# Kernel optimization log

Measured on AMD Instinct MI355X. Metric: run time of the kernel, lower is better.

The kernel has to match this reference:

```python
import jax, jax.numpy as jnp
import numpy as np
from jax import lax

T = 8
TAU = 2.0
V_TH = 1.0
V_RESET = 0.0
ALPHA = 2.0  # ATan surrogate width


@jax.custom_vjp
def spike(x):
    # Heaviside forward, ATan surrogate backward (spikingjelly surrogate.ATan)
    return (x >= 0.0).astype(x.dtype)

def _spike_fwd(x):
    return spike(x), x

def _spike_bwd(x, g):
    pi_half_alpha = jnp.asarray(np.pi / 2.0 * ALPHA, x.dtype)
    grad = (ALPHA / 2.0) / (1.0 + (pi_half_alpha * x) ** 2)
    return (g * grad,)

spike.defvjp(_spike_fwd, _spike_bwd)


def lif_multistep(x_seq):
    # x_seq: [T, ...]; hard-reset LIF with decay_input=True:
    #   v <- v + (x - (v - v_reset)) / tau ; s = H(v - v_th) ; v <- (1-s)*v + s*v_reset
    v0 = jnp.full(x_seq.shape[1:], V_RESET, x_seq.dtype)
    def step(v, x):
        v = v + (x - (v - V_RESET)) / TAU
        s = spike(v - V_TH)
        v = (1.0 - s) * v + s * V_RESET
        return v, s
    _, s_seq = lax.scan(step, v0, x_seq)
    return s_seq


def conv2d(x, w, b, stride):
    y = lax.conv_general_dilated(x, w, (stride, stride), 'VALID',
                                 dimension_numbers=('NCHW', 'OIHW', 'NCHW'))
    return y + b[None, :, None, None]


def seq_conv(x_seq, w, b, stride):
    # SeqToANNContainer: fold T into batch, run conv, unfold
    t, bsz = x_seq.shape[0], x_seq.shape[1]
    y = conv2d(x_seq.reshape((t * bsz,) + x_seq.shape[2:]), w, b, stride)
    return y.reshape((t, bsz) + y.shape[1:])


def setup_inputs() -> dict:
    key = jax.random.key(0)
    ks = jax.random.split(key, 12)
    s = 0.05
    return {
        'x':    jax.random.normal(ks[0], (512, 4, 84, 84), jnp.float32),
        'w1':   jax.random.normal(ks[1], (32, 4, 8, 8), jnp.float32) * s,
        'b1':   jax.random.normal(ks[2], (32,), jnp.float32) * s,
        'w2':   jax.random.normal(ks[3], (64, 32, 4, 4), jnp.float32) * s,
        'b2':   jax.random.normal(ks[4], (64,), jnp.float32) * s,
        'w3':   jax.random.normal(ks[5], (64, 64, 3, 3), jnp.float32) * s,
        'b3':   jax.random.normal(ks[6], (64,), jnp.float32) * s,
        'fw1':  jax.random.normal(ks[7], (512, 64 * 7 * 7), jnp.float32) * s,
        'fb1':  jax.random.normal(ks[8], (512,), jnp.float32) * s,
        'fw2':  jax.random.normal(ks[9], (6, 512), jnp.float32) * s,
        'fb2':  jax.random.normal(ks[10], (6,), jnp.float32) * s,
    }


def reference(x, w1, b1, w2, b2, w3, b3, fw1, fb1, fw2, fb2):
    # static conv, then replicate across T timesteps
    h = conv2d(x, w1, b1, 4)                      # [B,32,20,20]
    x_seq = jnp.broadcast_to(h[None], (T,) + h.shape)
    s = lif_multistep(x_seq)                      # [T,B,32,20,20]
    s = lif_multistep(seq_conv(s, w2, b2, 2))     # [T,B,64,9,9]
    s = lif_multistep(seq_conv(s, w3, b3, 1))     # [T,B,64,7,7]
    flat = s.reshape(T, s.shape[1], -1)           # [T,B,3136]
    s = lif_multistep(jnp.einsum('tbi,oi->tbo', flat, fw1) + fb1)  # [T,B,512]
    out = s.mean(axis=0)                          # [B,512]
    return out @ fw2.T + fb2                      # [B,6]
```

## Files before the change

### kernel.cpp

```cpp
#include <hip/hip_runtime.h>
#include <cstdint>

#define RFL(x) __builtin_amdgcn_readfirstlane(x)

static constexpr int B  = 512;
static constexpr int C0 = 4,  H0 = 84, W0 = 84;
static constexpr int C1 = 32, H1 = 20, W1 = 20, P1 = H1 * W1;
static constexpr int C2 = 64, H2 = 9,  W2 = 9,  P2 = H2 * W2;
static constexpr int C3 = 64, H3 = 7,  W3 = 7,  P3 = H3 * W3;
static constexpr int K  = C3 * P3;
static constexpr int O  = 512;
static constexpr int NJOB2 = B * P2;

static constexpr size_t OFF_S1   = 0;
static constexpr size_t OFF_S2   = 6553600;
static constexpr size_t OFF_S3   = OFF_S2 + 2654208;
static constexpr size_t OFF_W2T  = OFF_S3 + 1605632;
static constexpr size_t OFF_W3T  = OFF_W2T + 131072 + 256;
static constexpr size_t OFF_FW1T = OFF_W3T + 147456;
static constexpr size_t OFF_W1T  = OFF_FW1T + 6422528;
static constexpr size_t OFF_CNT  = OFF_W1T + 32768;
static constexpr size_t OFF_EVT  = OFF_CNT + (size_t)NJOB2 * 32;
static constexpr size_t WS_NEEDED = OFF_EVT + (size_t)NJOB2 * 1088;

__global__ void k_prep_w1(const float* __restrict__ w1, float* __restrict__ w1T) {
    int n = blockIdx.x * 256 + threadIdx.x;
    if (n >= 8192) return;
    int kx = n & 7, o = (n >> 3) & 7, ky = (n >> 6) & 7, ic = (n >> 9) & 3, o8 = n >> 11;
    int oc = o8 * 8 + o;
    w1T[n] = w1[((oc * 4 + ic) * 8 + ky) * 8 + kx];
}

__global__ void k_prep_w2(const float* __restrict__ w2, float* __restrict__ w2T) {
    int idx = blockIdx.x * 256 + threadIdx.x;
    if (idx >= 32768) {
        if (idx < 32768 + 64) w2T[idx] = 0.0f;
        return;
    }
    int oc = idx >> 9, r = idx & 511;
    int ic = r >> 4, ky = (r >> 2) & 3, kx = r & 3;
    w2T[((ky * 4 + kx) * 32 + ic) * 64 + oc] = w2[idx];
}

__global__ void k_prep_w3(const float* __restrict__ w3, float* __restrict__ w3T) {
    int idx = blockIdx.x * 256 + threadIdx.x;
    if (idx >= 64 * 64 * 9) return;
    int oc = idx / 576, r = idx - oc * 576;
    int ic = r / 9, rr = r - ic * 9;
    int ky = rr / 3, kx = rr - ky * 3;
    w3T[((ky * 3 + kx) * 64 + ic) * 64 + oc] = w3[idx];
}

__global__ __launch_bounds__(256) void k_prep_fw1(const float* __restrict__ fw1,
                                                  float* __restrict__ fw1T) {
    __shared__ float tile[64][65];
    int ot = blockIdx.x & 7;
    int it = blockIdx.x >> 3;
    int tr = threadIdx.x >> 6;
    int tc = threadIdx.x & 63;
    #pragma unroll
    for (int r = 0; r < 16; r++) {
        int ol = r * 4 + tr;
        tile[ol][tc] = fw1[(size_t)(ot * 64 + ol) * K + it * 64 + tc];
    }
    __syncthreads();
    #pragma unroll
    for (int r = 0; r < 16; r++) {
        int il = r * 4 + tr;
        fw1T[(size_t)(it * 64 + il) * O + ot * 64 + tc] = tile[tc][il];
    }
}

__global__ __launch_bounds__(256) void k_conv1(const float* __restrict__ x,
                                               const float* __restrict__ w1T,
                                               const float* __restrict__ b1,
                                               uint8_t* __restrict__ s1c) {
    int blk = blockIdx.x;
    int o8  = blk / 400;
    int rest = (blk - o8 * 400) * 256 + threadIdx.x;
    int img = rest / 200, pair = rest - img * 200;
    int oy  = pair / 10;
    int ox0 = (pair - oy * 10) * 2;
    const float* xb = x + (size_t)img * 28224 + (size_t)(oy * 4) * W0 + ox0 * 4;
    const float* wh = w1T + o8 * 2048;

    float acc[2][8];
    #pragma unroll
    for (int pp = 0; pp < 2; pp++)
        #pragma unroll
        for (int o = 0; o < 8; o++) acc[pp][o] = b1[o8 * 8 + o];

    #pragma unroll 1
    for (int ic = 0; ic < C0; ic++) {
        #pragma unroll 1
        for (int ky = 0; ky < 8; ky++) {
            const float* rp = xb + ic * 7056 + ky * W0;
            float4 a0 = *(const float4*)rp;
            float4 a1 = *(const float4*)(rp + 4);
            float4 a2 = *(const float4*)(rp + 8);
            float xv[12] = {a0.x, a0.y, a0.z, a0.w, a1.x, a1.y, a1.z, a1.w,
                            a2.x, a2.y, a2.z, a2.w};
            const float* wb = wh + (ic * 8 + ky) * 64;
            #pragma unroll
            for (int o = 0; o < 8; o++) {
                #pragma unroll
                for (int pp = 0; pp < 2; pp++) {
                    float s = acc[pp][o];
                    #pragma unroll
                    for (int kx = 0; kx < 8; kx++)
                        s = fmaf(wb[o * 8 + kx], xv[pp * 4 + kx], s);
                    acc[pp][o] = s;
                }
            }
        }
    }

    #pragma unroll
    for (int pp = 0; pp < 2; pp++) {
        uint32_t byc[8] = {0, 0, 0, 0, 0, 0, 0, 0};
        #pragma unroll
        for (int o = 0; o < 8; o++) {
            float h = acc[pp][o], v = 0.f;
            uint32_t mm = 0;
            #pragma unroll
            for (int t = 0; t < 8; t++) {
                v = v + (h - v) * 0.5f;
                bool sp = (v >= 1.0f);
                mm |= sp ? (1u << t) : 0u;
                v = sp ? 0.f : v;
            }
            uint32_t fs = mm & (0u - mm);
            #pragma unroll
            for (int c = 0; c < 8; c++) byc[c] |= ((fs >> c) & 1u) << o;
        }
        int pix = oy * W1 + ox0 + pp;
        uint8_t* op = s1c + (size_t)(img * P1 + pix) * 32 + o8;
        #pragma unroll
        for (int c = 0; c < 8; c++) op[c * 4] = (uint8_t)byc[c];
    }
}

__global__ __launch_bounds__(256) void k_evt(const uint8_t* __restrict__ s1c,
                                             uint32_t* __restrict__ cnt,
                                             uint16_t* __restrict__ evl) {
    int job = blockIdx.x * 256 + threadIdx.x;
    if (job >= NJOB2) return;
    int b = job / P2, pix = job - b * P2;
    int oy = pix / W2, ox = pix - oy * W2;
    uint16_t* out = evl + (size_t)job * 544;
    int k = 0;
    #pragma unroll 1
    for (int c = 0; c < 8; c++) {
        int start = k;
        #pragma unroll 1
        for (int pos = 0; pos < 16; pos++) {
            int ky = pos >> 2, kx = pos & 3;
            int ipix = (oy * 2 + ky) * W1 + ox * 2 + kx;
            uint32_t w = *(const uint32_t*)(s1c + (size_t)(b * P1 + ipix) * 32 + c * 4);
            while (w) {
                int i = __builtin_ctz(w);
                w &= w - 1;
                out[k++] = (uint16_t)((pos << 5) + i);
            }
        }
        while ((k - start) & 3) out[k++] = 512;
        cnt[job * 8 + c] = (uint32_t)(k - start);
    }
}

__global__ __launch_bounds__(256) void k_conv2_ev(const uint32_t* __restrict__ cnt,
                                                  const uint16_t* __restrict__ evl,
                                                  const float* __restrict__ w2T,
                                                  const float* __restrict__ b2,
                                                  uint8_t* __restrict__ s2p) {
    int wid = RFL(blockIdx.x * 4 + (threadIdx.x >> 6));
    int lane = threadIdx.x & 63;
    int b = wid / P2, pix = wid - b * P2;
    const uint32_t* evw = (const uint32_t*)(evl + (size_t)wid * 544);
    const uint32_t* cp  = cnt + wid * 8;
    float A[8];
    #pragma unroll
    for (int c = 0; c < 8; c++) A[c] = 0.f;
    int kw = 0;
    #define CLS(c)                                                            \
    {   int n = (int)cp[c];                                                   \
        for (int k = 0; k < n; k += 4) {                                      \
            uint32_t d0 = evw[kw], d1 = evw[kw + 1]; kw += 2;                 \
            float v0 = w2T[(d0 & 0xffffu) * 64 + lane];                       \
            float v1 = w2T[(d0 >> 16)    * 64 + lane];                        \
            float v2 = w2T[(d1 & 0xffffu) * 64 + lane];                       \
            float v3 = w2T[(d1 >> 16)    * 64 + lane];                        \
            A[c] += v0; A[c] += v1; A[c] += v2; A[c] += v3;                   \
        }                                                                     \
    }
    CLS(0) CLS(1) CLS(2) CLS(3) CLS(4) CLS(5) CLS(6) CLS(7)
    #undef CLS

    float y[8];
    y[0] = A[0];
    y[1] = A[0] + A[1];
    y[2] = A[0] + A[2];
    y[3] = A[0] + A[1] + A[3];
    y[4] = A[0] + A[4];
    y[5] = A[0] + A[1] + A[2] + A[5];
    y[6] = A[0] + A[6];
    y[7] = A[0] + A[1] + A[3] + A[7];

    float bo = b2[lane];
    uint32_t mout = 0;
    float v = 0.f;
    #pragma unroll
    for (int t = 0; t < 8; t++) {
        float yt = y[t] + bo;
        v = v + (yt - v) * 0.5f;
        bool sp = (v >= 1.0f);
        mout |= sp ? (1u << t) : 0u;
        v = sp ? 0.f : v;
    }
    unsigned long long* op = (unsigned long long*)(s2p + (size_t)(b * P2 + pix) * 64);
    #pragma unroll
    for (int t = 0; t < 8; t++) {
        unsigned long long bm = __ballot((mout >> t) & 1u);
        if (lane == 0) op[t] = bm;
    }
}

__global__ __launch_bounds__(256) void k_conv2_old(const uint8_t* __restrict__ s1c,
                                                   const float* __restrict__ w2T,
                                                   const float* __restrict__ b2,
                                                   uint8_t* __restrict__ s2p) {
    int wid = blockIdx.x * 4 + (threadIdx.x >> 6);
    int lane = threadIdx.x & 63;
    int b = wid / P2, pix = wid - b * P2;
    int oy = pix / W2, ox = pix - oy * W2;
    float A[8];
    #pragma unroll
    for (int c = 0; c < 8; c++) A[c] = 0.f;
    #pragma unroll
    for (int ky = 0; ky < 4; ky++) {
        #pragma unroll
        for (int kx = 0; kx < 4; kx++) {
            int mofs = RFL((b * P1 + (oy * 2 + ky) * W1 + (ox * 2 + kx)) * 32);
            const uint32_t* mp = (const uint32_t*)(s1c + mofs);
            const float* wp = w2T + (ky * 4 + kx) * 32 * 64 + lane;
            uint32_t w0 = mp[0], w1 = mp[1], w2 = mp[2], w3 = mp[3];
            uint32_t w4 = mp[4], w5 = mp[5], w6 = mp[6], w7 = mp[7];
            while (w0 | w1 | w2 | w3 | w4 | w5 | w6 | w7) {
                if (w0) { int i = __builtin_ctz(w0); w0 &= w0 - 1; A[0] += wp[i * 64]; }
                if (w1) { int i = __builtin_ctz(w1); w1 &= w1 - 1; A[1] += wp[i * 64]; }
                if (w2) { int i = __builtin_ctz(w2); w2 &= w2 - 1; A[2] += wp[i * 64]; }
                if (w3) { int i = __builtin_ctz(w3); w3 &= w3 - 1; A[3] += wp[i * 64]; }
                if (w4) { int i = __builtin_ctz(w4); w4 &= w4 - 1; A[4] += wp[i * 64]; }
                if (w5) { int i = __builtin_ctz(w5); w5 &= w5 - 1; A[5] += wp[i * 64]; }
                if (w6) { int i = __builtin_ctz(w6); w6 &= w6 - 1; A[6] += wp[i * 64]; }
                if (w7) { int i = __builtin_ctz(w7); w7 &= w7 - 1; A[7] += wp[i * 64]; }
            }
        }
    }
    float y[8];
    y[0] = A[0];
    y[1] = A[0] + A[1];
    y[2] = A[0] + A[2];
    y[3] = A[0] + A[1] + A[3];
    y[4] = A[0] + A[4];
    y[5] = A[0] + A[1] + A[2] + A[5];
    y[6] = A[0] + A[6];
    y[7] = A[0] + A[1] + A[3] + A[7];
    float bo = b2[lane];
    uint32_t mout = 0;
    float v = 0.f;
    #pragma unroll
    for (int t = 0; t < 8; t++) {
        float yt = y[t] + bo;
        v = v + (yt - v) * 0.5f;
        bool sp = (v >= 1.0f);
        mout |= sp ? (1u << t) : 0u;
        v = sp ? 0.f : v;
    }
    unsigned long long* op = (unsigned long long*)(s2p + (size_t)(b * P2 + pix) * 64);
    #pragma unroll
    for (int t = 0; t < 8; t++) {
        unsigned long long bm = __ballot((mout >> t) & 1u);
        if (lane == 0) op[t] = bm;
    }
}

__global__ __launch_bounds__(256) void k_conv3(const uint8_t* __restrict__ s2p,
                                               const float* __restrict__ w3T,
                                               const float* __restrict__ b3,
                                               uint8_t* __restrict__ s3m) {
    int wid = blockIdx.x * 4 + (threadIdx.x >> 6);
    int lane = threadIdx.x & 63;
    int b = wid / P3, pix = wid - b * P3;
    int oy = pix / W3, ox = pix - oy * W3;
    float A[8];
    #pragma unroll
    for (int t = 0; t < 8; t++) A[t] = 0.f;
    #pragma unroll
    for (int ky = 0; ky < 3; ky++) {
        #pragma unroll
        for (int kx = 0; kx < 3; kx++) {
            int mofs = RFL((b * P2 + (oy + ky) * W2 + (ox + kx)) * 64);
            const unsigned long long* mp = (const unsigned long long*)(s2p + mofs);
            const float* wp = w3T + (ky * 3 + kx) * 64 * 64 + lane;
            unsigned long long m0 = mp[0], m1 = mp[1], m2 = mp[2], m3 = mp[3];
            unsigned long long m4 = mp[4], m5 = mp[5], m6 = mp[6], m7 = mp[7];
            while (m0 | m1 | m2 | m3 | m4 | m5 | m6 | m7) {
                if (m0) { int i = __builtin_ctzll(m0); m0 &= m0 - 1; A[0] += wp[i * 64]; }
                if (m1) { int i = __builtin_ctzll(m1); m1 &= m1 - 1; A[1] += wp[i * 64]; }
                if (m2) { int i = __builtin_ctzll(m2); m2 &= m2 - 1; A[2] += wp[i * 64]; }
                if (m3) { int i = __builtin_ctzll(m3); m3 &= m3 - 1; A[3] += wp[i * 64]; }
                if (m4) { int i = __builtin_ctzll(m4); m4 &= m4 - 1; A[4] += wp[i * 64]; }
                if (m5) { int i = __builtin_ctzll(m5); m5 &= m5 - 1; A[5] += wp[i * 64]; }
                if (m6) { int i = __builtin_ctzll(m6); m6 &= m6 - 1; A[6] += wp[i * 64]; }
                if (m7) { int i = __builtin_ctzll(m7); m7 &= m7 - 1; A[7] += wp[i * 64]; }
            }
        }
    }
    float bo = b3[lane];
    uint32_t mout = 0;
    float v = 0.f;
    #pragma unroll
    for (int t = 0; t < 8; t++) {
        float y = A[t] + bo;
        v = v + (y - v) * 0.5f;
        bool sp = (v >= 1.0f);
        mout |= sp ? (1u << t) : 0u;
        v = sp ? 0.f : v;
    }
    s3m[(size_t)(b * P3 + pix) * 64 + lane] = (uint8_t)mout;
}

__global__ __launch_bounds__(256) void k_fc(const uint8_t* __restrict__ s3m,
                                            const float* __restrict__ fw1T,
                                            const float* __restrict__ fb1,
                                            const float* __restrict__ fw2,
                                            const float* __restrict__ fb2,
                                            float* __restrict__ out) {
    __shared__ float red[3][64][65];
    int b = blockIdx.x;
    int w = threadIdx.x >> 6;
    int lane = threadIdx.x & 63;
    float acc[8][8];
    #pragma unroll
    for (int j = 0; j < 8; j++)
        #pragma unroll
        for (int t = 0; t < 8; t++) acc[j][t] = 0.f;

    int ibeg = w * 784;
    for (int i0 = ibeg; i0 < ibeg + 784; i0 += 16) {
        int base = RFL(b * K + i0);
        const uint32_t* mp = (const uint32_t*)(s3m + base);
        #pragma unroll
        for (int d = 0; d < 4; d++) {
            uint32_t md = mp[d];
            if (md == 0) continue;
            #pragma unroll
            for (int q = 0; q < 4; q++) {
                uint32_t m = (md >> (q * 8)) & 0xffu;
                if (m == 0) continue;
                int i_our = i0 + d * 4 + q;
                int pix = i_our >> 6, c = i_our & 63;
                const float4* wp = (const float4*)(fw1T + (size_t)(c * 49 + pix) * O + lane * 8);
                float4 wa = wp[0], wb = wp[1];
                float wv[8] = {wa.x, wa.y, wa.z, wa.w, wb.x, wb.y, wb.z, wb.w};
                #pragma unroll
                for (int t = 0; t < 8; t++) {
                    if (m & (1u << t)) {
                        #pragma unroll
                        for (int j = 0; j < 8; j++) acc[j][t] += wv[j];
                    }
                }
            }
        }
    }

    if (w > 0) {
        #pragma unroll
        for (int j = 0; j < 8; j++)
            #pragma unroll
            for (int t = 0; t < 8; t++) red[w - 1][lane][j * 8 + t] = acc[j][t];
    }
    __syncthreads();
    if (w != 0) return;

    #pragma unroll
    for (int ww = 0; ww < 3; ww++)
        #pragma unroll
        for (int j = 0; j < 8; j++)
            #pragma unroll
            for (int t = 0; t < 8; t++) acc[j][t] += red[ww][lane][j * 8 + t];

    float msum[8];
    #pragma unroll
    for (int j = 0; j < 8; j++) {
        float yb = fb1[lane * 8 + j];
        float v = 0.f, cntt = 0.f;
        #pragma unroll
        for (int t = 0; t < 8; t++) {
            float y = acc[j][t] + yb;
            v = v + (y - v) * 0.5f;
            bool sp = (v >= 1.0f);
            cntt += sp ? 1.f : 0.f;
            v = sp ? 0.f : v;
        }
        msum[j] = cntt * 0.125f;
    }
    #pragma unroll
    for (int kk = 0; kk < 6; kk++) {
        const float* wr = fw2 + kk * O + lane * 8;
        float pv = 0.f;
        #pragma unroll
        for (int j = 0; j < 8; j++) pv += msum[j] * wr[j];
        #pragma unroll
        for (int off = 32; off > 0; off >>= 1) pv += __shfl_down(pv, off, 64);
        if (lane == 0) out[b * 6 + kk] = pv + fb2[kk];
    }
}

extern "C" void kernel_launch(void* const* d_in, const int* in_sizes, int n_in,
                              void* d_out, int out_size, void* d_ws, size_t ws_size,
                              hipStream_t stream) {
    const float* x   = (const float*)d_in[0];
    const float* w1  = (const float*)d_in[1];
    const float* b1  = (const float*)d_in[2];
    const float* w2  = (const float*)d_in[3];
    const float* b2  = (const float*)d_in[4];
    const float* w3  = (const float*)d_in[5];
    const float* b3  = (const float*)d_in[6];
    const float* fw1 = (const float*)d_in[7];
    const float* fb1 = (const float*)d_in[8];
    const float* fw2 = (const float*)d_in[9];
    const float* fb2 = (const float*)d_in[10];
    float* out = (float*)d_out;

    uint8_t*  ws   = (uint8_t*)d_ws;
    uint8_t*  s1c  = ws + OFF_S1;
    uint8_t*  s2p  = ws + OFF_S2;
    uint8_t*  s3m  = ws + OFF_S3;
    float*    w2T  = (float*)(ws + OFF_W2T);
    float*    w3T  = (float*)(ws + OFF_W3T);
    float*    fw1T = (float*)(ws + OFF_FW1T);
    float*    w1T  = (float*)(ws + OFF_W1T);
    uint32_t* cnt  = (uint32_t*)(ws + OFF_CNT);
    uint16_t* evl  = (uint16_t*)(ws + OFF_EVT);

    hipLaunchKernelGGL(k_prep_w1,  dim3(32),    dim3(256), 0, stream, w1, w1T);
    hipLaunchKernelGGL(k_prep_w2,  dim3(129),   dim3(256), 0, stream, w2, w2T);
    hipLaunchKernelGGL(k_prep_w3,  dim3(144),   dim3(256), 0, stream, w3, w3T);
    hipLaunchKernelGGL(k_prep_fw1, dim3(392),   dim3(256), 0, stream, fw1, fw1T);
    hipLaunchKernelGGL(k_conv1,    dim3(1600),  dim3(256), 0, stream, x, w1T, b1, s1c);
    if (ws_size >= WS_NEEDED) {
        hipLaunchKernelGGL(k_evt,      dim3(162),   dim3(256), 0, stream, s1c, cnt, evl);
        hipLaunchKernelGGL(k_conv2_ev, dim3(10368), dim3(256), 0, stream, cnt, evl, w2T, b2, s2p);
    } else {
        hipLaunchKernelGGL(k_conv2_old, dim3(10368), dim3(256), 0, stream, s1c, w2T, b2, s2p);
    }
    hipLaunchKernelGGL(k_conv3,    dim3(6272),  dim3(256), 0, stream, s2p, w3T, b3, s3m);
    hipLaunchKernelGGL(k_fc,       dim3(512),   dim3(256), 0, stream, s3m, fw1T, fb1, fw2, fb2, out);
}
```

Measured before the change: 194.4 us.

## Parallelize event-list build across channel groups and unroll conv2 gather by eight

The event-list builder now gives each of the 8 channel groups of an output pixel its own thread. Each thread first popcounts its spikes, then uses a segmented shuffle prefix sum to find its write offset, and launches 8x more blocks. Groups are padded to multiples of 8 instead of 4, so the conv2 event kernel can issue 8 weight gathers per iteration for more memory-level parallelism. The per-job event buffer grows, and the extra padding adds wasted dummy gathers against a zero row.

```diff
diff --git a/kernel.cpp b/kernel.cpp
--- a/kernel.cpp
+++ b/kernel.cpp
@@ -21,7 +21,7 @@
 static constexpr size_t OFF_W1T  = OFF_FW1T + 6422528;
 static constexpr size_t OFF_CNT  = OFF_W1T + 32768;
 static constexpr size_t OFF_EVT  = OFF_CNT + (size_t)NJOB2 * 32;
-static constexpr size_t WS_NEEDED = OFF_EVT + (size_t)NJOB2 * 1088;
+static constexpr size_t WS_NEEDED = OFF_EVT + (size_t)NJOB2 * 1152;
 
 __global__ void k_prep_w1(const float* __restrict__ w1, float* __restrict__ w1T) {
     int n = blockIdx.x * 256 + threadIdx.x;
@@ -143,29 +143,42 @@
 __global__ __launch_bounds__(256) void k_evt(const uint8_t* __restrict__ s1c,
                                              uint32_t* __restrict__ cnt,
                                              uint16_t* __restrict__ evl) {
-    int job = blockIdx.x * 256 + threadIdx.x;
-    if (job >= NJOB2) return;
+    int tid = threadIdx.x;
+    int job = blockIdx.x * 32 + (tid >> 3);
+    int c   = tid & 7;
     int b = job / P2, pix = job - b * P2;
     int oy = pix / W2, ox = pix - oy * W2;
-    uint16_t* out = evl + (size_t)job * 544;
+    const uint8_t* sb = s1c + (size_t)b * P1 * 32 + c * 4;
+
+    int count = 0;
+    #pragma unroll
+    for (int pos = 0; pos < 16; pos++) {
+        int ipix = (oy * 2 + (pos >> 2)) * W1 + ox * 2 + (pos & 3);
+        count += __popc(*(const uint32_t*)(sb + (size_t)ipix * 32));
+    }
+    int padded = (count + 7) & ~7;
+
+    int incl = padded;
+    #pragma unroll
+    for (int d = 1; d < 8; d <<= 1) {
+        int t = __shfl_up(incl, d, 8);
+        if ((tid & 7) >= d) incl += t;
+    }
+    uint16_t* out = evl + (size_t)job * 576 + (incl - padded);
+
     int k = 0;
     #pragma unroll 1
-    for (int c = 0; c < 8; c++) {
-        int start = k;
-        #pragma unroll 1
-        for (int pos = 0; pos < 16; pos++) {
-            int ky = pos >> 2, kx = pos & 3;
-            int ipix = (oy * 2 + ky) * W1 + ox * 2 + kx;
-            uint32_t w = *(const uint32_t*)(s1c + (size_t)(b * P1 + ipix) * 32 + c * 4);
-            while (w) {
-                int i = __builtin_ctz(w);
-                w &= w - 1;
-                out[k++] = (uint16_t)((pos << 5) + i);
-            }
-        }
-        while ((k - start) & 3) out[k++] = 512;
-        cnt[job * 8 + c] = (uint32_t)(k - start);
-    }
+    for (int pos = 0; pos < 16; pos++) {
+        int ipix = (oy * 2 + (pos >> 2)) * W1 + ox * 2 + (pos & 3);
+        uint32_t w = *(const uint32_t*)(sb + (size_t)ipix * 32);
+        while (w) {
+            int i = __builtin_ctz(w);
+            w &= w - 1;
+            out[k++] = (uint16_t)((pos << 5) + i);
+        }
+    }
+    while (k < padded) out[k++] = 512;
+    cnt[job * 8 + c] = (uint32_t)padded;
 }
 
 __global__ __launch_bounds__(256) void k_conv2_ev(const uint32_t* __restrict__ cnt,
@@ -176,7 +189,7 @@
     int wid = RFL(blockIdx.x * 4 + (threadIdx.x >> 6));
     int lane = threadIdx.x & 63;
     int b = wid / P2, pix = wid - b * P2;
-    const uint32_t* evw = (const uint32_t*)(evl + (size_t)wid * 544);
+    const uint32_t* evw = (const uint32_t*)(evl + (size_t)wid * 576);
     const uint32_t* cp  = cnt + wid * 8;
     float A[8];
     #pragma unroll
@@ -184,13 +197,19 @@
     int kw = 0;
     #define CLS(c)                                                            \
     {   int n = (int)cp[c];                                                   \
-        for (int k = 0; k < n; k += 4) {                                      \
-            uint32_t d0 = evw[kw], d1 = evw[kw + 1]; kw += 2;                 \
+        for (int k = 0; k < n; k += 8) {                                      \
+            uint32_t d0 = evw[kw], d1 = evw[kw + 1];                          \
+            uint32_t d2 = evw[kw + 2], d3 = evw[kw + 3]; kw += 4;             \
             float v0 = w2T[(d0 & 0xffffu) * 64 + lane];                       \
             float v1 = w2T[(d0 >> 16)    * 64 + lane];                        \
             float v2 = w2T[(d1 & 0xffffu) * 64 + lane];                       \
             float v3 = w2T[(d1 >> 16)    * 64 + lane];                        \
+            float v4 = w2T[(d2 & 0xffffu) * 64 + lane];                       \
+            float v5 = w2T[(d2 >> 16)    * 64 + lane];                        \
+            float v6 = w2T[(d3 & 0xffffu) * 64 + lane];                       \
+            float v7 = w2T[(d3 >> 16)    * 64 + lane];                        \
             A[c] += v0; A[c] += v1; A[c] += v2; A[c] += v3;                   \
+            A[c] += v4; A[c] += v5; A[c] += v6; A[c] += v7;                   \
         }                                                                     \
     }
     CLS(0) CLS(1) CLS(2) CLS(3) CLS(4) CLS(5) CLS(6) CLS(7)
@@ -451,7 +470,7 @@
     hipLaunchKernelGGL(k_prep_fw1, dim3(392),   dim3(256), 0, stream, fw1, fw1T);
     hipLaunchKernelGGL(k_conv1,    dim3(1600),  dim3(256), 0, stream, x, w1T, b1, s1c);
     if (ws_size >= WS_NEEDED) {
-        hipLaunchKernelGGL(k_evt,      dim3(162),   dim3(256), 0, stream, s1c, cnt, evl);
+        hipLaunchKernelGGL(k_evt,      dim3(1296),  dim3(256), 0, stream, s1c, cnt, evl);
         hipLaunchKernelGGL(k_conv2_ev, dim3(10368), dim3(256), 0, stream, cnt, evl, w2T, b2, s2p);
     } else {
         hipLaunchKernelGGL(k_conv2_old, dim3(10368), dim3(256), 0, stream, s1c, w2T, b2, s2p);
```

Measured after the change: 172.5 us. 1.13x faster.
